# Kernel tuning notes

Measured on AMD Instinct MI355X. Metric: run time of the kernel, lower is better.

Reference implementation:

```python
import jax, jax.numpy as jnp
import numpy as np

D_MODEL = 1024
H = 16
DK = D_MODEL // H  # 64
BLK = 128
TAU = 1.0
EPS = 1e-12


def setup_inputs() -> dict:
    key = jax.random.key(0)
    ks = jax.random.split(key, 5)
    B, N = 1, 2048
    shp = (B, N, D_MODEL)
    q = jax.random.normal(ks[0], shp, dtype=jnp.float32)
    k = jax.random.normal(ks[1], shp, dtype=jnp.float32)
    v = jax.random.normal(ks[2], shp, dtype=jnp.float32)
    dO = jax.random.normal(ks[3], shp, dtype=jnp.float32)
    Tb = N // BLK  # 16 blocks per side
    block_sparse_mask = jax.random.randint(ks[4], (Tb, Tb), 0, 2, dtype=jnp.int32)
    return {"q": q, "k": k, "v": v, "dO": dO, "block_sparse_mask": block_sparse_mask}


def reference(q, k, v, dO, block_sparse_mask):
    B, N, _ = q.shape
    T = N // BLK  # number of blocks along sequence
    scale = TAU / np.sqrt(DK).astype(np.float32)

    def split(x):
        # (B,N,d_model) -> (B,H,T,BLK,DK)
        return x.reshape(B, N, H, DK).transpose(0, 2, 1, 3).reshape(B, H, T, BLK, DK)

    qb, kb, vb, dOb = split(q), split(k), split(v), split(dO)

    # block scores: (B,H,Ti,Tj,Br,Bc)
    S = jnp.einsum('bhipd,bhjqd->bhijpq', qb, kb) * scale
    # per-block (local) softmax normalization, exactly as in the source
    m = jnp.max(S, axis=-1, keepdims=True)
    P = jnp.exp(S - m)
    l = jnp.sum(P, axis=-1, keepdims=True)
    Pn = P / (l + EPS)

    dA = jnp.einsum('bhipd,bhjqd->bhijpq', dOb, vb)
    row_dot = jnp.sum(dA * Pn, axis=-1, keepdims=True)
    dS = Pn * (dA - row_dot)

    # block-sparse skipping: skipped (i,j) blocks contribute nothing
    bm = block_sparse_mask.astype(Pn.dtype)[None, None, :, :, None, None]
    Pn = Pn * bm
    dS = dS * bm

    dV = jnp.einsum('bhijpq,bhipd->bhjqd', Pn, dOb)
    dQ = jnp.einsum('bhijpq,bhjqd->bhipd', dS, kb) * scale
    dK = jnp.einsum('bhijpq,bhipd->bhjqd', dS, qb) * scale

    def merge(x):
        # (B,H,T,BLK,DK) -> (B,N,d_model)
        return x.reshape(B, H, N, DK).transpose(0, 2, 1, 3).reshape(B, N, D_MODEL)

    return (merge(dQ), merge(dK), merge(dV))
```

## Files before the change

kernel.cpp:

```cpp
#include <hip/hip_runtime.h>

#define DMODEL 1024
#define NHEAD  16
#define DKD    64
#define BLK    128
#define TB     16
#define SCALEF 0.125f

typedef __attribute__((ext_vector_type(8))) short bf16x8;
typedef __attribute__((ext_vector_type(4))) float f32x4;

#define MFMA16(A, B, C) __builtin_amdgcn_mfma_f32_16x16x32_bf16(A, B, C, 0, 0, 0)

__device__ __forceinline__ ushort bfc(float x) {
  union { float f; unsigned u; } c; c.f = x;
  const unsigned u = c.u;
  return (ushort)((u + 0x7FFFu + ((u >> 16) & 1u)) >> 16);
}

__device__ __forceinline__ bf16x8 frag(const ushort* T, int r, int c, int st) {
  return *reinterpret_cast<const bf16x8*>(T + ((r * st + c) ^ ((r & 7) << 3)));
}

__device__ __forceinline__ void stageR(ushort* T, const float* __restrict__ g,
                                       float sc, int tid) {
#pragma unroll
  for (int it = 0; it < 4; ++it) {
    const int idx = tid + 512 * it;
    const int r = idx >> 4, d4 = idx & 15;
    const float4 f = *reinterpret_cast<const float4*>(g + r * DMODEL + 4 * d4);
    ushort4 u;
    u.x = bfc(f.x * sc); u.y = bfc(f.y * sc); u.z = bfc(f.z * sc); u.w = bfc(f.w * sc);
    *reinterpret_cast<ushort4*>(T + ((r * 64 + 4 * d4) ^ ((r & 7) << 3))) = u;
  }
}

__device__ __forceinline__ void stageT(ushort* T, const float* __restrict__ g,
                                       float sc, int tid) {
#pragma unroll
  for (int it = 0; it < 2; ++it) {
    const int idx = tid + 512 * it;
    const int rp = idx >> 4, d4 = idx & 15;
    const float4 fa = *reinterpret_cast<const float4*>(g + (2 * rp) * DMODEL + 4 * d4);
    const float4 fb = *reinterpret_cast<const float4*>(g + (2 * rp + 1) * DMODEL + 4 * d4);
    const float a4[4] = {fa.x, fa.y, fa.z, fa.w};
    const float b4[4] = {fb.x, fb.y, fb.z, fb.w};
#pragma unroll
    for (int kkk = 0; kkk < 4; ++kkk) {
      const int d = 4 * d4 + kkk;
      ushort2 u; u.x = bfc(a4[kkk] * sc); u.y = bfc(b4[kkk] * sc);
      *reinterpret_cast<ushort2*>(T + ((d * 128 + 2 * rp) ^ ((d & 7) << 3))) = u;
    }
  }
}

__global__ void __launch_bounds__(512, 2)
bwd_all(const float* __restrict__ q, const float* __restrict__ kk,
        const float* __restrict__ v, const float* __restrict__ dOg,
        const int* __restrict__ mask,
        float* __restrict__ dQ, float* __restrict__ dK, float* __restrict__ dV) {
  __shared__ ushort sm[49152];
  const int tid = threadIdx.x;
  const int w = tid >> 6, l = tid & 63;
  const int l15 = l & 15, lg = l >> 4;
  const int pw = w * 16;
  const int bid = blockIdx.x;
  const int role = bid >> 8;
  const int h = (bid >> 4) & 15;
  const int blk = bid & 15;
  const f32x4 zz = {0.f, 0.f, 0.f, 0.f};

  if (role == 0) {
    const float* gq = q   + (size_t)(blk * BLK) * DMODEL + h * DKD;
    const float* go = dOg + (size_t)(blk * BLK) * DMODEL + h * DKD;
    stageR(sm + 0,    gq, 1.f, tid);
    stageR(sm + 8192, go, 1.f, tid);
    f32x4 accQ[4] = {zz, zz, zz, zz};

    for (int j = 0; j < TB; ++j) {
      if (!mask[blk * TB + j]) continue;
      const float* gk = kk + (size_t)(j * BLK) * DMODEL + h * DKD;
      const float* gv = v  + (size_t)(j * BLK) * DMODEL + h * DKD;
      stageR(sm + 16384, gk, SCALEF, tid);
      stageR(sm + 24576, gv, 1.f, tid);
      stageT(sm + 32768, gk, SCALEF, tid);
      __syncthreads();

      f32x4 ST[8]  = {zz, zz, zz, zz, zz, zz, zz, zz};
      f32x4 dAT[8] = {zz, zz, zz, zz, zz, zz, zz, zz};
#pragma unroll
      for (int kb = 0; kb < 2; ++kb) {
        const int c = kb * 32 + lg * 8;
        const bf16x8 bq = frag(sm + 0,    pw + l15, c, 64);
        const bf16x8 bo = frag(sm + 8192, pw + l15, c, 64);
#pragma unroll
        for (int mf = 0; mf < 8; ++mf) {
          ST[mf]  = MFMA16(frag(sm + 16384, mf * 16 + l15, c, 64), bq, ST[mf]);
          dAT[mf] = MFMA16(frag(sm + 24576, mf * 16 + l15, c, 64), bo, dAT[mf]);
        }
      }

      float mx = -1e30f;
#pragma unroll
      for (int mf = 0; mf < 8; ++mf)
#pragma unroll
        for (int r = 0; r < 4; ++r) mx = fmaxf(mx, ST[mf][r]);
      mx = fmaxf(mx, __shfl_xor(mx, 16));
      mx = fmaxf(mx, __shfl_xor(mx, 32));
      float ss = 0.f;
#pragma unroll
      for (int mf = 0; mf < 8; ++mf)
#pragma unroll
        for (int r = 0; r < 4; ++r) { const float e = __expf(ST[mf][r] - mx); ST[mf][r] = e; ss += e; }
      ss += __shfl_xor(ss, 16);
      ss += __shfl_xor(ss, 32);
      const float inv = 1.f / (ss + 1e-12f);
      float rd = 0.f;
#pragma unroll
      for (int mf = 0; mf < 8; ++mf)
#pragma unroll
        for (int r = 0; r < 4; ++r) { const float pn = ST[mf][r] * inv; ST[mf][r] = pn; rd += pn * dAT[mf][r]; }
      rd += __shfl_xor(rd, 16);
      rd += __shfl_xor(rd, 32);
#pragma unroll
      for (int mf = 0; mf < 8; ++mf)
#pragma unroll
        for (int r = 0; r < 4; ++r) dAT[mf][r] = ST[mf][r] * (dAT[mf][r] - rd);

      __syncthreads();

      const int p = pw + l15;
#pragma unroll
      for (int mf = 0; mf < 8; ++mf) {
        ushort4 u;
        u.x = bfc(dAT[mf][0]); u.y = bfc(dAT[mf][1]);
        u.z = bfc(dAT[mf][2]); u.w = bfc(dAT[mf][3]);
        *reinterpret_cast<ushort4*>(
            sm + 16384 + ((p * 128 + mf * 16 + lg * 4) ^ ((p & 7) << 3))) = u;
      }
      __syncthreads();

#pragma unroll
      for (int kb = 0; kb < 4; ++kb) {
        const int c = kb * 32 + lg * 8;
        const bf16x8 a = frag(sm + 16384, pw + l15, c, 128);
#pragma unroll
        for (int nf = 0; nf < 4; ++nf)
          accQ[nf] = MFMA16(a, frag(sm + 32768, nf * 16 + l15, c, 128), accQ[nf]);
      }
      __syncthreads();
    }

#pragma unroll
    for (int nf = 0; nf < 4; ++nf)
#pragma unroll
      for (int r = 0; r < 4; ++r)
        dQ[(size_t)(blk * BLK + pw + lg * 4 + r) * DMODEL + h * DKD + nf * 16 + l15] =
            accQ[nf][r];

  } else {
    const int jb = blk;
    stageR(sm + 0,    kk + (size_t)(jb * BLK) * DMODEL + h * DKD, 1.f, tid);
    stageR(sm + 8192, v  + (size_t)(jb * BLK) * DMODEL + h * DKD, 1.f, tid);
    f32x4 accK[4] = {zz, zz, zz, zz};
    f32x4 accV[4] = {zz, zz, zz, zz};

    for (int i = 0; i < TB; ++i) {
      if (!mask[i * TB + jb]) continue;
      const float* gq = q   + (size_t)(i * BLK) * DMODEL + h * DKD;
      const float* go = dOg + (size_t)(i * BLK) * DMODEL + h * DKD;
      stageR(sm + 16384, gq, SCALEF, tid);
      stageR(sm + 24576, go, 1.f, tid);
      stageT(sm + 32768, gq, SCALEF, tid);
      stageT(sm + 40960, go, 1.f, tid);
      __syncthreads();

      f32x4 S[8]  = {zz, zz, zz, zz, zz, zz, zz, zz};
      f32x4 dA[8] = {zz, zz, zz, zz, zz, zz, zz, zz};
#pragma unroll
      for (int kb = 0; kb < 2; ++kb) {
        const int c = kb * 32 + lg * 8;
        const bf16x8 aq = frag(sm + 16384, pw + l15, c, 64);
        const bf16x8 ao = frag(sm + 24576, pw + l15, c, 64);
#pragma unroll
        for (int nf = 0; nf < 8; ++nf) {
          S[nf]  = MFMA16(aq, frag(sm + 0,    nf * 16 + l15, c, 64), S[nf]);
          dA[nf] = MFMA16(ao, frag(sm + 8192, nf * 16 + l15, c, 64), dA[nf]);
        }
      }

#pragma unroll
      for (int r = 0; r < 4; ++r) {
        float mx = -1e30f;
#pragma unroll
        for (int nf = 0; nf < 8; ++nf) mx = fmaxf(mx, S[nf][r]);
        mx = fmaxf(mx, __shfl_xor(mx, 1));
        mx = fmaxf(mx, __shfl_xor(mx, 2));
        mx = fmaxf(mx, __shfl_xor(mx, 4));
        mx = fmaxf(mx, __shfl_xor(mx, 8));
        float ss = 0.f;
#pragma unroll
        for (int nf = 0; nf < 8; ++nf) { const float e = __expf(S[nf][r] - mx); S[nf][r] = e; ss += e; }
        ss += __shfl_xor(ss, 1);
        ss += __shfl_xor(ss, 2);
        ss += __shfl_xor(ss, 4);
        ss += __shfl_xor(ss, 8);
        const float inv = 1.f / (ss + 1e-12f);
        float rd = 0.f;
#pragma unroll
        for (int nf = 0; nf < 8; ++nf) { const float pn = S[nf][r] * inv; S[nf][r] = pn; rd += pn * dA[nf][r]; }
        rd += __shfl_xor(rd, 1);
        rd += __shfl_xor(rd, 2);
        rd += __shfl_xor(rd, 4);
        rd += __shfl_xor(rd, 8);
#pragma unroll
        for (int nf = 0; nf < 8; ++nf) dA[nf][r] = S[nf][r] * (dA[nf][r] - rd);
      }

      __syncthreads();

#pragma unroll
      for (int nf = 0; nf < 8; ++nf) {
        const int c = nf * 16 + l15;
        ushort4 u;
        u.x = bfc(S[nf][0]); u.y = bfc(S[nf][1]); u.z = bfc(S[nf][2]); u.w = bfc(S[nf][3]);
        *reinterpret_cast<ushort4*>(
            sm + 16384 + ((c * 128 + pw + lg * 4) ^ ((c & 7) << 3))) = u;
      }
      __syncthreads();

#pragma unroll
      for (int kb = 0; kb < 4; ++kb) {
        const int c = kb * 32 + lg * 8;
        const bf16x8 a = frag(sm + 16384, pw + l15, c, 128);
#pragma unroll
        for (int nf = 0; nf < 4; ++nf)
          accV[nf] = MFMA16(a, frag(sm + 40960, nf * 16 + l15, c, 128), accV[nf]);
      }
      __syncthreads();

#pragma unroll
      for (int nf = 0; nf < 8; ++nf) {
        const int c = nf * 16 + l15;
        ushort4 u;
        u.x = bfc(dA[nf][0]); u.y = bfc(dA[nf][1]); u.z = bfc(dA[nf][2]); u.w = bfc(dA[nf][3]);
        *reinterpret_cast<ushort4*>(
            sm + 16384 + ((c * 128 + pw + lg * 4) ^ ((c & 7) << 3))) = u;
      }
      __syncthreads();

#pragma unroll
      for (int kb = 0; kb < 4; ++kb) {
        const int c = kb * 32 + lg * 8;
        const bf16x8 a = frag(sm + 16384, pw + l15, c, 128);
#pragma unroll
        for (int nf = 0; nf < 4; ++nf)
          accK[nf] = MFMA16(a, frag(sm + 32768, nf * 16 + l15, c, 128), accK[nf]);
      }
      __syncthreads();
    }

#pragma unroll
    for (int nf = 0; nf < 4; ++nf)
#pragma unroll
      for (int r = 0; r < 4; ++r) {
        const size_t row = (size_t)(jb * BLK + pw + lg * 4 + r) * DMODEL + h * DKD + nf * 16 + l15;
        dK[row] = accK[nf][r];
        dV[row] = accV[nf][r];
      }
  }
}

extern "C" void kernel_launch(void* const* d_in, const int* in_sizes, int n_in,
                              void* d_out, int out_size, void* d_ws, size_t ws_size,
                              hipStream_t stream) {
  const float* q  = (const float*)d_in[0];
  const float* k  = (const float*)d_in[1];
  const float* v  = (const float*)d_in[2];
  const float* dO = (const float*)d_in[3];
  const int* mask = (const int*)d_in[4];
  float* out = (float*)d_out;
  float* dQ = out;
  float* dK = out + (size_t)2048 * DMODEL;
  float* dV = out + (size_t)2 * 2048 * DMODEL;

  bwd_all<<<2 * NHEAD * TB, 512, 0, stream>>>(q, k, v, dO, mask, dQ, dK, dV);
}
```

Before: 120.8 us.

## Halve block to 256 threads with 32 rows per wave and register-held Q/dO fragments

The block shrinks from 512 to 256 threads, and each wave now owns 32 rows, so every B fragment read from LDS feeds two MFMAs. Q and dO A-fragments are loaded straight from global memory into registers instead of being staged in LDS. The transposed staging now uses a shuffle-based 4x4 transpose and writes a new interleaved layout. Hardware bf16 packing replaces the manual rounding. LDS use falls from 96KB to 64KB. The risks are higher register pressure, fewer waves to hide latency, and the dK/dV path re-staging its own K/V tiles inside every loop iteration.

Result: slower. 278.5 us (+130.6%).

```diff
diff --git a/kernel.cpp b/kernel.cpp
--- a/kernel.cpp
+++ b/kernel.cpp
@@ -1,4 +1,5 @@
 #include <hip/hip_runtime.h>
+#include <hip/hip_bf16.h>
 
 #define DMODEL 1024
 #define NHEAD  16
@@ -10,60 +11,105 @@
 typedef __attribute__((ext_vector_type(8))) short bf16x8;
 typedef __attribute__((ext_vector_type(4))) float f32x4;
 
-#define MFMA16(A, B, C) __builtin_amdgcn_mfma_f32_16x16x32_bf16(A, B, C, 0, 0, 0)
-
-__device__ __forceinline__ ushort bfc(float x) {
-  union { float f; unsigned u; } c; c.f = x;
-  const unsigned u = c.u;
-  return (ushort)((u + 0x7FFFu + ((u >> 16) & 1u)) >> 16);
-}
-
-__device__ __forceinline__ bf16x8 frag(const ushort* T, int r, int c, int st) {
-  return *reinterpret_cast<const bf16x8*>(T + ((r * st + c) ^ ((r & 7) << 3)));
-}
-
-__device__ __forceinline__ void stageR(ushort* T, const float* __restrict__ g,
-                                       float sc, int tid) {
-#pragma unroll
-  for (int it = 0; it < 4; ++it) {
-    const int idx = tid + 512 * it;
+#define MFMA(A, B, C) __builtin_amdgcn_mfma_f32_16x16x32_bf16(A, B, C, 0, 0, 0)
+
+union U8 { bf16x8 v; ushort u[8]; ushort2 u2[4]; ushort4 u4[2]; };
+
+__device__ __forceinline__ ushort2 pk2(float a, float b) {
+  union { __hip_bfloat162 h; ushort2 u; } c;
+  c.h = __float22bfloat162_rn(make_float2(a, b));
+  return c.u;
+}
+
+__device__ __forceinline__ bf16x8 frag64(const ushort* T, int r, int c) {
+  return *reinterpret_cast<const bf16x8*>(T + ((r * 64 + c) ^ ((r & 7) << 3)));
+}
+__device__ __forceinline__ bf16x8 frag128(const ushort* T, int r, int c) {
+  return *reinterpret_cast<const bf16x8*>(T + ((r * 128 + c) ^ ((r & 7) << 3)));
+}
+__device__ __forceinline__ bf16x8 fragT2(const ushort* T, int d, int r0) {
+  U8 x;
+  x.u4[0] = *reinterpret_cast<const ushort4*>(T + (r0 >> 2) * 256 + d * 4);
+  x.u4[1] = *reinterpret_cast<const ushort4*>(T + (r0 >> 2) * 256 + 256 + d * 4);
+  return x.v;
+}
+__device__ __forceinline__ bf16x8 gfrag(const float* __restrict__ g, float sc) {
+  const float4 fa = *reinterpret_cast<const float4*>(g);
+  const float4 fb = *reinterpret_cast<const float4*>(g + 4);
+  U8 x;
+  x.u2[0] = pk2(fa.x * sc, fa.y * sc);
+  x.u2[1] = pk2(fa.z * sc, fa.w * sc);
+  x.u2[2] = pk2(fb.x * sc, fb.y * sc);
+  x.u2[3] = pk2(fb.z * sc, fb.w * sc);
+  return x.v;
+}
+
+__device__ __forceinline__ void stage_row(ushort* T, const float* __restrict__ g,
+                                          float sc, int tid) {
+#pragma unroll
+  for (int it = 0; it < 8; ++it) {
+    const int idx = tid + 256 * it;
     const int r = idx >> 4, d4 = idx & 15;
     const float4 f = *reinterpret_cast<const float4*>(g + r * DMODEL + 4 * d4);
-    ushort4 u;
-    u.x = bfc(f.x * sc); u.y = bfc(f.y * sc); u.z = bfc(f.z * sc); u.w = bfc(f.w * sc);
+    const ushort2 lo = pk2(f.x * sc, f.y * sc);
+    const ushort2 hi = pk2(f.z * sc, f.w * sc);
+    ushort4 u; u.x = lo.x; u.y = lo.y; u.z = hi.x; u.w = hi.y;
     *reinterpret_cast<ushort4*>(T + ((r * 64 + 4 * d4) ^ ((r & 7) << 3))) = u;
   }
 }
 
-__device__ __forceinline__ void stageT(ushort* T, const float* __restrict__ g,
-                                       float sc, int tid) {
-#pragma unroll
-  for (int it = 0; it < 2; ++it) {
-    const int idx = tid + 512 * it;
-    const int rp = idx >> 4, d4 = idx & 15;
-    const float4 fa = *reinterpret_cast<const float4*>(g + (2 * rp) * DMODEL + 4 * d4);
-    const float4 fb = *reinterpret_cast<const float4*>(g + (2 * rp + 1) * DMODEL + 4 * d4);
-    const float a4[4] = {fa.x, fa.y, fa.z, fa.w};
-    const float b4[4] = {fb.x, fb.y, fb.z, fb.w};
-#pragma unroll
-    for (int kkk = 0; kkk < 4; ++kkk) {
-      const int d = 4 * d4 + kkk;
-      ushort2 u; u.x = bfc(a4[kkk] * sc); u.y = bfc(b4[kkk] * sc);
-      *reinterpret_cast<ushort2*>(T + ((d * 128 + 2 * rp) ^ ((d & 7) << 3))) = u;
+template <bool ALSO_ROW>
+__device__ __forceinline__ void stage_T(ushort* T, ushort* Trow,
+                                        const float* __restrict__ g, float sc, int tid) {
+  const int a = (tid >> 4) & 3;
+#pragma unroll
+  for (int it = 0; it < 8; ++it) {
+    const int idx = tid + 256 * it;
+    const int r = idx >> 4, d4 = idx & 15;
+    const float4 f = *reinterpret_cast<const float4*>(g + r * DMODEL + 4 * d4);
+    const float w0 = f.x * sc, w1 = f.y * sc, w2 = f.z * sc, w3 = f.w * sc;
+    if constexpr (ALSO_ROW) {
+      const ushort2 lo = pk2(w0, w1);
+      const ushort2 hi = pk2(w2, w3);
+      ushort4 u; u.x = lo.x; u.y = lo.y; u.z = hi.x; u.w = hi.y;
+      *reinterpret_cast<ushort4*>(Trow + ((r * 64 + 4 * d4) ^ ((r & 7) << 3))) = u;
     }
+    const float s0 = __shfl_xor(w1, 16), s1 = __shfl_xor(w0, 16);
+    const float s2 = __shfl_xor(w3, 16), s3 = __shfl_xor(w2, 16);
+    const float u0 = (a & 1) ? s0 : w0;
+    const float u1 = (a & 1) ? w1 : s1;
+    const float u2 = (a & 1) ? s2 : w2;
+    const float u3 = (a & 1) ? w3 : s3;
+    const float t0 = __shfl_xor(u2, 32), t1 = __shfl_xor(u3, 32);
+    const float t2 = __shfl_xor(u0, 32), t3 = __shfl_xor(u1, 32);
+    const float z0 = (a & 2) ? t0 : u0;
+    const float z1 = (a & 2) ? t1 : u1;
+    const float z2 = (a & 2) ? u2 : t2;
+    const float z3 = (a & 2) ? u3 : t3;
+    const int d = 4 * d4 + a, R0 = r - a;
+    const ushort2 lo = pk2(z0, z1);
+    const ushort2 hi = pk2(z2, z3);
+    ushort4 o; o.x = lo.x; o.y = lo.y; o.z = hi.x; o.w = hi.y;
+    *reinterpret_cast<ushort4*>(T + (R0 >> 2) * 256 + d * 4) = o;
   }
 }
 
-__global__ void __launch_bounds__(512, 2)
+__global__ void __launch_bounds__(256, 2)
 bwd_all(const float* __restrict__ q, const float* __restrict__ kk,
         const float* __restrict__ v, const float* __restrict__ dOg,
         const int* __restrict__ mask,
         float* __restrict__ dQ, float* __restrict__ dK, float* __restrict__ dV) {
-  __shared__ ushort sm[49152];
+  __shared__ ushort sm[32768];
+  ushort* smK = sm;
+  ushort* smV = sm + 8192;
+  ushort* smX = sm;
+  ushort* smT0 = sm + 16384;
+  ushort* smT1 = sm + 24576;
   const int tid = threadIdx.x;
-  const int w = tid >> 6, l = tid & 63;
+  const int l = tid & 63;
   const int l15 = l & 15, lg = l >> 4;
-  const int pw = w * 16;
+  const int w = tid >> 6;
+  const int pw = w * 32;
   const int bid = blockIdx.x;
   const int role = bid >> 8;
   const int h = (bid >> 4) & 15;
@@ -71,203 +117,257 @@
   const f32x4 zz = {0.f, 0.f, 0.f, 0.f};
 
   if (role == 0) {
-    const float* gq = q   + (size_t)(blk * BLK) * DMODEL + h * DKD;
-    const float* go = dOg + (size_t)(blk * BLK) * DMODEL + h * DKD;
-    stageR(sm + 0,    gq, 1.f, tid);
-    stageR(sm + 8192, go, 1.f, tid);
-    f32x4 accQ[4] = {zz, zz, zz, zz};
+    bf16x8 bq[2][2], bo[2][2];
+#pragma unroll
+    for (int t = 0; t < 2; ++t)
+#pragma unroll
+      for (int kb = 0; kb < 2; ++kb) {
+        const size_t row = (size_t)(blk * BLK + pw + 16 * t + l15) * DMODEL + h * DKD + kb * 32 + lg * 8;
+        bq[t][kb] = gfrag(q + row, 1.f);
+        bo[t][kb] = gfrag(dOg + row, 1.f);
+      }
+    f32x4 accQ[2][4] = {{zz, zz, zz, zz}, {zz, zz, zz, zz}};
 
     for (int j = 0; j < TB; ++j) {
       if (!mask[blk * TB + j]) continue;
-      const float* gk = kk + (size_t)(j * BLK) * DMODEL + h * DKD;
-      const float* gv = v  + (size_t)(j * BLK) * DMODEL + h * DKD;
-      stageR(sm + 16384, gk, SCALEF, tid);
-      stageR(sm + 24576, gv, 1.f, tid);
-      stageT(sm + 32768, gk, SCALEF, tid);
-      __syncthreads();
-
-      f32x4 ST[8]  = {zz, zz, zz, zz, zz, zz, zz, zz};
-      f32x4 dAT[8] = {zz, zz, zz, zz, zz, zz, zz, zz};
+      stage_T<true>(smT0, smK, kk + (size_t)(j * BLK) * DMODEL + h * DKD, SCALEF, tid);
+      stage_row(smV, v + (size_t)(j * BLK) * DMODEL + h * DKD, 1.f, tid);
+      __syncthreads();
+
+      f32x4 ST[2][8], dAT[2][8];
+#pragma unroll
+      for (int t = 0; t < 2; ++t)
+#pragma unroll
+        for (int mf = 0; mf < 8; ++mf) { ST[t][mf] = zz; dAT[t][mf] = zz; }
 #pragma unroll
       for (int kb = 0; kb < 2; ++kb) {
-        const int c = kb * 32 + lg * 8;
-        const bf16x8 bq = frag(sm + 0,    pw + l15, c, 64);
-        const bf16x8 bo = frag(sm + 8192, pw + l15, c, 64);
+        const int ck = kb * 32 + lg * 8;
 #pragma unroll
         for (int mf = 0; mf < 8; ++mf) {
-          ST[mf]  = MFMA16(frag(sm + 16384, mf * 16 + l15, c, 64), bq, ST[mf]);
-          dAT[mf] = MFMA16(frag(sm + 24576, mf * 16 + l15, c, 64), bo, dAT[mf]);
-        }
-      }
-
-      float mx = -1e30f;
-#pragma unroll
-      for (int mf = 0; mf < 8; ++mf)
-#pragma unroll
-        for (int r = 0; r < 4; ++r) mx = fmaxf(mx, ST[mf][r]);
-      mx = fmaxf(mx, __shfl_xor(mx, 16));
-      mx = fmaxf(mx, __shfl_xor(mx, 32));
-      float ss = 0.f;
-#pragma unroll
-      for (int mf = 0; mf < 8; ++mf)
-#pragma unroll
-        for (int r = 0; r < 4; ++r) { const float e = __expf(ST[mf][r] - mx); ST[mf][r] = e; ss += e; }
-      ss += __shfl_xor(ss, 16);
-      ss += __shfl_xor(ss, 32);
-      const float inv = 1.f / (ss + 1e-12f);
-      float rd = 0.f;
-#pragma unroll
-      for (int mf = 0; mf < 8; ++mf)
-#pragma unroll
-        for (int r = 0; r < 4; ++r) { const float pn = ST[mf][r] * inv; ST[mf][r] = pn; rd += pn * dAT[mf][r]; }
-      rd += __shfl_xor(rd, 16);
-      rd += __shfl_xor(rd, 32);
-#pragma unroll
-      for (int mf = 0; mf < 8; ++mf)
-#pragma unroll
-        for (int r = 0; r < 4; ++r) dAT[mf][r] = ST[mf][r] * (dAT[mf][r] - rd);
-
-      __syncthreads();
-
-      const int p = pw + l15;
-#pragma unroll
-      for (int mf = 0; mf < 8; ++mf) {
-        ushort4 u;
-        u.x = bfc(dAT[mf][0]); u.y = bfc(dAT[mf][1]);
-        u.z = bfc(dAT[mf][2]); u.w = bfc(dAT[mf][3]);
-        *reinterpret_cast<ushort4*>(
-            sm + 16384 + ((p * 128 + mf * 16 + lg * 4) ^ ((p & 7) << 3))) = u;
-      }
-      __syncthreads();
-
-#pragma unroll
-      for (int kb = 0; kb < 4; ++kb) {
-        const int c = kb * 32 + lg * 8;
-        const bf16x8 a = frag(sm + 16384, pw + l15, c, 128);
-#pragma unroll
-        for (int nf = 0; nf < 4; ++nf)
-          accQ[nf] = MFMA16(a, frag(sm + 32768, nf * 16 + l15, c, 128), accQ[nf]);
+          const bf16x8 ak = frag64(smK, mf * 16 + l15, ck);
+          const bf16x8 av = frag64(smV, mf * 16 + l15, ck);
+          ST[0][mf] = MFMA(ak, bq[0][kb], ST[0][mf]);
+          ST[1][mf] = MFMA(ak, bq[1][kb], ST[1][mf]);
+          dAT[0][mf] = MFMA(av, bo[0][kb], dAT[0][mf]);
+          dAT[1][mf] = MFMA(av, bo[1][kb], dAT[1][mf]);
+        }
+      }
+#pragma unroll
+      for (int t = 0; t < 2; ++t) {
+        float mx = -1e30f;
+#pragma unroll
+        for (int mf = 0; mf < 8; ++mf)
+#pragma unroll
+          for (int r = 0; r < 4; ++r) mx = fmaxf(mx, ST[t][mf][r]);
+        mx = fmaxf(mx, __shfl_xor(mx, 16));
+        mx = fmaxf(mx, __shfl_xor(mx, 32));
+        float ss = 0.f;
+#pragma unroll
+        for (int mf = 0; mf < 8; ++mf)
+#pragma unroll
+          for (int r = 0; r < 4; ++r) { const float e = __expf(ST[t][mf][r] - mx); ST[t][mf][r] = e; ss += e; }
+        ss += __shfl_xor(ss, 16);
+        ss += __shfl_xor(ss, 32);
+        const float inv = 1.f / (ss + 1e-12f);
+        float rd = 0.f;
+#pragma unroll
+        for (int mf = 0; mf < 8; ++mf)
+#pragma unroll
+          for (int r = 0; r < 4; ++r) { const float pn = ST[t][mf][r] * inv; ST[t][mf][r] = pn; rd += pn * dAT[t][mf][r]; }
+        rd += __shfl_xor(rd, 16);
+        rd += __shfl_xor(rd, 32);
+#pragma unroll
+        for (int mf = 0; mf < 8; ++mf)
+#pragma unroll
+          for (int r = 0; r < 4; ++r) dAT[t][mf][r] = ST[t][mf][r] * (dAT[t][mf][r] - rd);
+      }
+      __syncthreads();
+#pragma unroll
+      for (int t = 0; t < 2; ++t) {
+        const int p = pw + 16 * t + l15;
+#pragma unroll
+        for (int mf = 0; mf < 8; ++mf) {
+          const ushort2 lo = pk2(dAT[t][mf][0], dAT[t][mf][1]);
+          const ushort2 hi = pk2(dAT[t][mf][2], dAT[t][mf][3]);
+          ushort4 u; u.x = lo.x; u.y = lo.y; u.z = hi.x; u.w = hi.y;
+          *reinterpret_cast<ushort4*>(smX + ((p * 128 + mf * 16 + 4 * lg) ^ ((p & 7) << 3))) = u;
+        }
+      }
+      __syncthreads();
+#pragma unroll
+      for (int kc = 0; kc < 4; ++kc) {
+        const int cc = kc * 32 + lg * 8;
+        const bf16x8 a0 = frag128(smX, pw + l15, cc);
+        const bf16x8 a1 = frag128(smX, pw + 16 + l15, cc);
+#pragma unroll
+        for (int nf = 0; nf < 4; ++nf) {
+          const bf16x8 b = fragT2(smT0, nf * 16 + l15, cc);
+          accQ[0][nf] = MFMA(a0, b, accQ[0][nf]);
+          accQ[1][nf] = MFMA(a1, b, accQ[1][nf]);
+        }
       }
       __syncthreads();
     }
-
-#pragma unroll
-    for (int nf = 0; nf < 4; ++nf)
-#pragma unroll
-      for (int r = 0; r < 4; ++r)
-        dQ[(size_t)(blk * BLK + pw + lg * 4 + r) * DMODEL + h * DKD + nf * 16 + l15] =
-            accQ[nf][r];
+#pragma unroll
+    for (int t = 0; t < 2; ++t)
+#pragma unroll
+      for (int nf = 0; nf < 4; ++nf)
+#pragma unroll
+        for (int r = 0; r < 4; ++r)
+          dQ[(size_t)(blk * BLK + pw + 16 * t + lg * 4 + r) * DMODEL + h * DKD + nf * 16 + l15] = accQ[t][nf][r];
 
   } else {
     const int jb = blk;
-    stageR(sm + 0,    kk + (size_t)(jb * BLK) * DMODEL + h * DKD, 1.f, tid);
-    stageR(sm + 8192, v  + (size_t)(jb * BLK) * DMODEL + h * DKD, 1.f, tid);
-    f32x4 accK[4] = {zz, zz, zz, zz};
-    f32x4 accV[4] = {zz, zz, zz, zz};
+    f32x4 accK[2][4] = {{zz, zz, zz, zz}, {zz, zz, zz, zz}};
+    f32x4 accV[2][4] = {{zz, zz, zz, zz}, {zz, zz, zz, zz}};
 
     for (int i = 0; i < TB; ++i) {
       if (!mask[i * TB + jb]) continue;
-      const float* gq = q   + (size_t)(i * BLK) * DMODEL + h * DKD;
-      const float* go = dOg + (size_t)(i * BLK) * DMODEL + h * DKD;
-      stageR(sm + 16384, gq, SCALEF, tid);
-      stageR(sm + 24576, go, 1.f, tid);
-      stageT(sm + 32768, gq, SCALEF, tid);
-      stageT(sm + 40960, go, 1.f, tid);
-      __syncthreads();
-
-      f32x4 S[8]  = {zz, zz, zz, zz, zz, zz, zz, zz};
-      f32x4 dA[8] = {zz, zz, zz, zz, zz, zz, zz, zz};
+      stage_row(smK, kk + (size_t)(jb * BLK) * DMODEL + h * DKD, SCALEF, tid);
+      stage_row(smV, v + (size_t)(jb * BLK) * DMODEL + h * DKD, 1.f, tid);
+      stage_T<false>(smT0, nullptr, q + (size_t)(i * BLK) * DMODEL + h * DKD, SCALEF, tid);
+      stage_T<false>(smT1, nullptr, dOg + (size_t)(i * BLK) * DMODEL + h * DKD, 1.f, tid);
+      bf16x8 aq[2][2];
+#pragma unroll
+      for (int Mt = 0; Mt < 2; ++Mt)
+#pragma unroll
+        for (int kb = 0; kb < 2; ++kb)
+          aq[Mt][kb] = gfrag(q + (size_t)(i * BLK + pw + 16 * Mt + l15) * DMODEL + h * DKD + kb * 32 + lg * 8, 1.f);
+      __syncthreads();
+
+      f32x4 S[2][8];
+#pragma unroll
+      for (int Mt = 0; Mt < 2; ++Mt)
+#pragma unroll
+        for (int nf = 0; nf < 8; ++nf) S[Mt][nf] = zz;
 #pragma unroll
       for (int kb = 0; kb < 2; ++kb) {
-        const int c = kb * 32 + lg * 8;
-        const bf16x8 aq = frag(sm + 16384, pw + l15, c, 64);
-        const bf16x8 ao = frag(sm + 24576, pw + l15, c, 64);
+        const int ck = kb * 32 + lg * 8;
 #pragma unroll
         for (int nf = 0; nf < 8; ++nf) {
-          S[nf]  = MFMA16(aq, frag(sm + 0,    nf * 16 + l15, c, 64), S[nf]);
-          dA[nf] = MFMA16(ao, frag(sm + 8192, nf * 16 + l15, c, 64), dA[nf]);
-        }
-      }
-
-#pragma unroll
-      for (int r = 0; r < 4; ++r) {
-        float mx = -1e30f;
-#pragma unroll
-        for (int nf = 0; nf < 8; ++nf) mx = fmaxf(mx, S[nf][r]);
-        mx = fmaxf(mx, __shfl_xor(mx, 1));
-        mx = fmaxf(mx, __shfl_xor(mx, 2));
-        mx = fmaxf(mx, __shfl_xor(mx, 4));
-        mx = fmaxf(mx, __shfl_xor(mx, 8));
-        float ss = 0.f;
-#pragma unroll
-        for (int nf = 0; nf < 8; ++nf) { const float e = __expf(S[nf][r] - mx); S[nf][r] = e; ss += e; }
-        ss += __shfl_xor(ss, 1);
-        ss += __shfl_xor(ss, 2);
-        ss += __shfl_xor(ss, 4);
-        ss += __shfl_xor(ss, 8);
-        const float inv = 1.f / (ss + 1e-12f);
-        float rd = 0.f;
-#pragma unroll
-        for (int nf = 0; nf < 8; ++nf) { const float pn = S[nf][r] * inv; S[nf][r] = pn; rd += pn * dA[nf][r]; }
-        rd += __shfl_xor(rd, 1);
-        rd += __shfl_xor(rd, 2);
-        rd += __shfl_xor(rd, 4);
-        rd += __shfl_xor(rd, 8);
-#pragma unroll
-        for (int nf = 0; nf < 8; ++nf) dA[nf][r] = S[nf][r] * (dA[nf][r] - rd);
-      }
-
-      __syncthreads();
-
-#pragma unroll
-      for (int nf = 0; nf < 8; ++nf) {
-        const int c = nf * 16 + l15;
-        ushort4 u;
-        u.x = bfc(S[nf][0]); u.y = bfc(S[nf][1]); u.z = bfc(S[nf][2]); u.w = bfc(S[nf][3]);
-        *reinterpret_cast<ushort4*>(
-            sm + 16384 + ((c * 128 + pw + lg * 4) ^ ((c & 7) << 3))) = u;
-      }
-      __syncthreads();
-
-#pragma unroll
-      for (int kb = 0; kb < 4; ++kb) {
-        const int c = kb * 32 + lg * 8;
-        const bf16x8 a = frag(sm + 16384, pw + l15, c, 128);
-#pragma unroll
-        for (int nf = 0; nf < 4; ++nf)
-          accV[nf] = MFMA16(a, frag(sm + 40960, nf * 16 + l15, c, 128), accV[nf]);
-      }
-      __syncthreads();
-
-#pragma unroll
-      for (int nf = 0; nf < 8; ++nf) {
-        const int c = nf * 16 + l15;
-        ushort4 u;
-        u.x = bfc(dA[nf][0]); u.y = bfc(dA[nf][1]); u.z = bfc(dA[nf][2]); u.w = bfc(dA[nf][3]);
-        *reinterpret_cast<ushort4*>(
-            sm + 16384 + ((c * 128 + pw + lg * 4) ^ ((c & 7) << 3))) = u;
-      }
-      __syncthreads();
-
-#pragma unroll
-      for (int kb = 0; kb < 4; ++kb) {
-        const int c = kb * 32 + lg * 8;
-        const bf16x8 a = frag(sm + 16384, pw + l15, c, 128);
-#pragma unroll
-        for (int nf = 0; nf < 4; ++nf)
-          accK[nf] = MFMA16(a, frag(sm + 32768, nf * 16 + l15, c, 128), accK[nf]);
+          const bf16x8 bk = frag64(smK, nf * 16 + l15, ck);
+          S[0][nf] = MFMA(aq[0][kb], bk, S[0][nf]);
+          S[1][nf] = MFMA(aq[1][kb], bk, S[1][nf]);
+        }
+      }
+#pragma unroll
+      for (int Mt = 0; Mt < 2; ++Mt)
+#pragma unroll
+        for (int r = 0; r < 4; ++r) {
+          float mx = -1e30f;
+#pragma unroll
+          for (int nf = 0; nf < 8; ++nf) mx = fmaxf(mx, S[Mt][nf][r]);
+          mx = fmaxf(mx, __shfl_xor(mx, 1));
+          mx = fmaxf(mx, __shfl_xor(mx, 2));
+          mx = fmaxf(mx, __shfl_xor(mx, 4));
+          mx = fmaxf(mx, __shfl_xor(mx, 8));
+          float ss = 0.f;
+#pragma unroll
+          for (int nf = 0; nf < 8; ++nf) { const float e = __expf(S[Mt][nf][r] - mx); S[Mt][nf][r] = e; ss += e; }
+          ss += __shfl_xor(ss, 1); ss += __shfl_xor(ss, 2);
+          ss += __shfl_xor(ss, 4); ss += __shfl_xor(ss, 8);
+          const float inv = 1.f / (ss + 1e-12f);
+#pragma unroll
+          for (int nf = 0; nf < 8; ++nf) S[Mt][nf][r] *= inv;
+        }
+      bf16x8 ao[2][2];
+#pragma unroll
+      for (int Mt = 0; Mt < 2; ++Mt)
+#pragma unroll
+        for (int kb = 0; kb < 2; ++kb)
+          ao[Mt][kb] = gfrag(dOg + (size_t)(i * BLK + pw + 16 * Mt + l15) * DMODEL + h * DKD + kb * 32 + lg * 8, 1.f);
+      f32x4 dA[2][8];
+#pragma unroll
+      for (int Mt = 0; Mt < 2; ++Mt)
+#pragma unroll
+        for (int nf = 0; nf < 8; ++nf) dA[Mt][nf] = zz;
+#pragma unroll
+      for (int kb = 0; kb < 2; ++kb) {
+        const int ck = kb * 32 + lg * 8;
+#pragma unroll
+        for (int nf = 0; nf < 8; ++nf) {
+          const bf16x8 bv = frag64(smV, nf * 16 + l15, ck);
+          dA[0][nf] = MFMA(ao[0][kb], bv, dA[0][nf]);
+          dA[1][nf] = MFMA(ao[1][kb], bv, dA[1][nf]);
+        }
+      }
+#pragma unroll
+      for (int Mt = 0; Mt < 2; ++Mt)
+#pragma unroll
+        for (int r = 0; r < 4; ++r) {
+          float rd = 0.f;
+#pragma unroll
+          for (int nf = 0; nf < 8; ++nf) rd += S[Mt][nf][r] * dA[Mt][nf][r];
+          rd += __shfl_xor(rd, 1); rd += __shfl_xor(rd, 2);
+          rd += __shfl_xor(rd, 4); rd += __shfl_xor(rd, 8);
+#pragma unroll
+          for (int nf = 0; nf < 8; ++nf) dA[Mt][nf][r] = S[Mt][nf][r] * (dA[Mt][nf][r] - rd);
+        }
+      __syncthreads();
+
+#pragma unroll
+      for (int Mt = 0; Mt < 2; ++Mt) {
+        const int p0 = pw + 16 * Mt + 4 * lg;
+#pragma unroll
+        for (int nf = 0; nf < 8; ++nf) {
+          const int c = nf * 16 + l15;
+          const ushort2 lo = pk2(S[Mt][nf][0], S[Mt][nf][1]);
+          const ushort2 hi = pk2(S[Mt][nf][2], S[Mt][nf][3]);
+          ushort4 u; u.x = lo.x; u.y = lo.y; u.z = hi.x; u.w = hi.y;
+          *reinterpret_cast<ushort4*>(smX + ((c * 128 + p0) ^ ((c & 7) << 3))) = u;
+        }
+      }
+      __syncthreads();
+#pragma unroll
+      for (int kp = 0; kp < 4; ++kp) {
+        const int pp = kp * 32 + lg * 8;
+        const bf16x8 a0 = frag128(smX, pw + l15, pp);
+        const bf16x8 a1 = frag128(smX, pw + 16 + l15, pp);
+#pragma unroll
+        for (int nf = 0; nf < 4; ++nf) {
+          const bf16x8 b = fragT2(smT1, nf * 16 + l15, pp);
+          accV[0][nf] = MFMA(a0, b, accV[0][nf]);
+          accV[1][nf] = MFMA(a1, b, accV[1][nf]);
+        }
+      }
+      __syncthreads();
+#pragma unroll
+      for (int Mt = 0; Mt < 2; ++Mt) {
+        const int p0 = pw + 16 * Mt + 4 * lg;
+#pragma unroll
+        for (int nf = 0; nf < 8; ++nf) {
+          const int c = nf * 16 + l15;
+          const ushort2 lo = pk2(dA[Mt][nf][0], dA[Mt][nf][1]);
+          const ushort2 hi = pk2(dA[Mt][nf][2], dA[Mt][nf][3]);
+          ushort4 u; u.x = lo.x; u.y = lo.y; u.z = hi.x; u.w = hi.y;
+          *reinterpret_cast<ushort4*>(smX + ((c * 128 + p0) ^ ((c & 7) << 3))) = u;
+        }
+      }
+      __syncthreads();
+#pragma unroll
+      for (int kp = 0; kp < 4; ++kp) {
+        const int pp = kp * 32 + lg * 8;
+        const bf16x8 a0 = frag128(smX, pw + l15, pp);
+        const bf16x8 a1 = frag128(smX, pw + 16 + l15, pp);
+#pragma unroll
+        for (int nf = 0; nf < 4; ++nf) {
+          const bf16x8 b = fragT2(smT0, nf * 16 + l15, pp);
+          accK[0][nf] = MFMA(a0, b, accK[0][nf]);
+          accK[1][nf] = MFMA(a1, b, accK[1][nf]);
+        }
       }
       __syncthreads();
     }
-
-#pragma unroll
-    for (int nf = 0; nf < 4; ++nf)
-#pragma unroll
-      for (int r = 0; r < 4; ++r) {
-        const size_t row = (size_t)(jb * BLK + pw + lg * 4 + r) * DMODEL + h * DKD + nf * 16 + l15;
-        dK[row] = accK[nf][r];
-        dV[row] = accV[nf][r];
-      }
+#pragma unroll
+    for (int Mt = 0; Mt < 2; ++Mt)
+#pragma unroll
+      for (int nf = 0; nf < 4; ++nf)
+#pragma unroll
+        for (int r = 0; r < 4; ++r) {
+          const size_t rowo = (size_t)(jb * BLK + pw + 16 * Mt + lg * 4 + r) * DMODEL + h * DKD + nf * 16 + l15;
+          dK[rowo] = accK[Mt][nf][r];
+          dV[rowo] = accV[Mt][nf][r];
+        }
   }
 }
 
@@ -284,5 +384,5 @@
   float* dK = out + (size_t)2048 * DMODEL;
   float* dV = out + (size_t)2 * 2048 * DMODEL;
 
-  bwd_all<<<2 * NHEAD * TB, 512, 0, stream>>>(q, k, v, dO, mask, dQ, dK, dV);
-}
+  bwd_all<<<2 * NHEAD * TB, 256, 0, stream>>>(q, k, v, dO, mask, dQ, dK, dV);
+}
```
